# Optimization experiments

Hardware: AMD Instinct MI355X
Metric: run time of the kernel (lower is better)

The kernel has to match this reference:

```python
import jax, jax.numpy as jnp
import numpy as np

B, S, D = 4, 4096, 64

def setup_inputs() -> dict:
    key = jax.random.key(0)
    k1, k2, k3 = jax.random.split(key, 3)
    inputs = jax.random.normal(k1, (B, S, D), dtype=jnp.float32)
    rotation = jax.random.normal(k2, (D, D), dtype=jnp.float32)
    entangle = jax.random.normal(k3, (D, D), dtype=jnp.float32)
    return {"inputs": inputs, "rotation": rotation, "entangle": entangle}

def reference(inputs, rotation, entangle):
    # query/key projections: [B,S,D] @ [D,D] -> [B,S,D]
    query = jnp.einsum('bsd,de->bse', inputs, rotation)
    key = jnp.einsum('bsd,de->bse', inputs, entangle)
    scale = 1.0 / jnp.sqrt(jnp.float32(inputs.shape[-1]))
    # scores: [B,S,S] softmax over last axis
    scores = jax.nn.softmax(jnp.einsum('bqd,bkd->bqk', query, key) * scale, axis=-1)
    # values are the raw inputs (no value projection)
    return jnp.einsum('bqk,bkd->bqd', scores, inputs)
```

## Files before the change

### kernel.cpp

```cpp
#include <hip/hip_runtime.h>
#include <hip/hip_fp16.h>

#define BB 4
#define SS 4096
#define DD 64
#define NSPLIT 4
#define KT_PER (SS / 64 / NSPLIT)

typedef _Float16 half8 __attribute__((ext_vector_type(8)));
typedef _Float16 half4 __attribute__((ext_vector_type(4)));
typedef __fp16 fp16x2 __attribute__((ext_vector_type(2)));
typedef float floatx4 __attribute__((ext_vector_type(4)));

__global__ __launch_bounds__(256) void proj_kernel(
    const float* __restrict__ X, const float* __restrict__ R, const float* __restrict__ E,
    _Float16* __restrict__ Qhi, _Float16* __restrict__ Qlo,
    _Float16* __restrict__ Khi, _Float16* __restrict__ Klo,
    _Float16* __restrict__ Vt)
{
    __shared__ float Rs[64][64];
    __shared__ float Es[64][64];
    __shared__ float Xs[16][68];
    int t = threadIdx.x;
    long rowbase = (long)blockIdx.x * 16;

    for (int j = 0; j < 4; ++j) {
        int idx = j * 256 + t;
        int r = idx >> 4;
        int c = (idx & 15) * 4;
        *(float4*)&Rs[r][c] = ((const float4*)R)[idx];
        *(float4*)&Es[r][c] = ((const float4*)E)[idx];
    }
    *(float4*)&Xs[t >> 4][(t & 15) * 4] = ((const float4*)(X + rowbase * 64))[t];
    __syncthreads();

    int row = t >> 4;
    int c0 = (t & 15) * 4;
    float q[4] = {0.f, 0.f, 0.f, 0.f}, k[4] = {0.f, 0.f, 0.f, 0.f};
#pragma unroll 4
    for (int d = 0; d < 64; ++d) {
        float x = Xs[row][d];
        float4 rv = *(const float4*)&Rs[d][c0];
        float4 ev = *(const float4*)&Es[d][c0];
        q[0] = fmaf(x, rv.x, q[0]); q[1] = fmaf(x, rv.y, q[1]);
        q[2] = fmaf(x, rv.z, q[2]); q[3] = fmaf(x, rv.w, q[3]);
        k[0] = fmaf(x, ev.x, k[0]); k[1] = fmaf(x, ev.y, k[1]);
        k[2] = fmaf(x, ev.z, k[2]); k[3] = fmaf(x, ev.w, k[3]);
    }
    long gq = (rowbase + row) * 64 + c0;
    half4 qh, ql, kh, kl;
    for (int j = 0; j < 4; ++j) {
        _Float16 h = (_Float16)q[j];
        qh[j] = h; ql[j] = (_Float16)(q[j] - (float)h);
        h = (_Float16)k[j];
        kh[j] = h; kl[j] = (_Float16)(k[j] - (float)h);
    }
    *(half4*)(Qhi + gq) = qh; *(half4*)(Qlo + gq) = ql;
    *(half4*)(Khi + gq) = kh; *(half4*)(Klo + gq) = kl;

    int d = t >> 2;
    int si = (t & 3) * 4;
    int b = (int)(rowbase >> 12);
    int sbase = (int)(rowbase & 4095);
    half4 v;
    for (int j = 0; j < 4; ++j) v[j] = (_Float16)Xs[si + j][d];
    *(half4*)(Vt + ((long)(b * 64 + d)) * SS + sbase + si) = v;
}

#define L2E 1.44269504088896340736f
#define PD 72

__global__ __launch_bounds__(256, 4) void attn_partial(
    const _Float16* __restrict__ Qhi, const _Float16* __restrict__ Qlo,
    const _Float16* __restrict__ Khi, const _Float16* __restrict__ Klo,
    const _Float16* __restrict__ Vt,
    float* __restrict__ Op, float* __restrict__ Mp, float* __restrict__ Lp)
{
    __shared__ _Float16 Ksh[64][PD];
    __shared__ _Float16 Ksl[64][PD];
    __shared__ _Float16 Vs[64][PD];
    __shared__ _Float16 Ps[4][16][PD];

    int t = threadIdx.x;
    int wave = t >> 6;
    int lane = t & 63;
    int l15 = lane & 15;
    int quad = lane >> 4;
    int split = blockIdx.y;
    int b = blockIdx.z;
    int q0 = blockIdx.x * 64 + wave * 16;

    long qrow = ((long)b * SS + q0 + l15) * DD;
    half8 qa0h = *(const half8*)(Qhi + qrow + quad * 8);
    half8 qa1h = *(const half8*)(Qhi + qrow + 32 + quad * 8);
    half8 qa0l = *(const half8*)(Qlo + qrow + quad * 8);
    half8 qa1l = *(const half8*)(Qlo + qrow + 32 + quad * 8);

    floatx4 o[4];
    for (int i = 0; i < 4; ++i) o[i] = (floatx4){0.f, 0.f, 0.f, 0.f};
    float m_q = -1e30f;
    float l_q = 0.f;

    const float scale = 0.125f * L2E;

    int rr = t >> 2;
    int cc = (t & 3) * 16;
    long kbase = ((long)b * SS + rr) * DD + cc;
    long vbase = ((long)b * 64 + rr) * SS + cc;

    int kt = split * KT_PER;
    uint4 rh0, rh1, rl0, rl1, rv0, rv1;
    {
        const uint4* khsrc = (const uint4*)(Khi + kbase + (long)kt * 64 * DD);
        rh0 = khsrc[0]; rh1 = khsrc[1];
        const uint4* klsrc = (const uint4*)(Klo + kbase + (long)kt * 64 * DD);
        rl0 = klsrc[0]; rl1 = klsrc[1];
        const uint4* vsrc = (const uint4*)(Vt + vbase + kt * 64);
        rv0 = vsrc[0]; rv1 = vsrc[1];
    }

    for (int i = 0; i < KT_PER; ++i) {
        if (i > 0) __syncthreads();
        {
            uint4* khdst = (uint4*)&Ksh[rr][cc];
            khdst[0] = rh0; khdst[1] = rh1;
            uint4* kldst = (uint4*)&Ksl[rr][cc];
            kldst[0] = rl0; kldst[1] = rl1;
            uint4* vdst = (uint4*)&Vs[rr][cc];
            vdst[0] = rv0; vdst[1] = rv1;
        }
        __syncthreads();

        int ktn = (i + 1 < KT_PER) ? (kt + 1) : kt;
        {
            const uint4* khsrc = (const uint4*)(Khi + kbase + (long)ktn * 64 * DD);
            rh0 = khsrc[0]; rh1 = khsrc[1];
            const uint4* klsrc = (const uint4*)(Klo + kbase + (long)ktn * 64 * DD);
            rl0 = klsrc[0]; rl1 = klsrc[1];
            const uint4* vsrc = (const uint4*)(Vt + vbase + ktn * 64);
            rv0 = vsrc[0]; rv1 = vsrc[1];
        }
        kt = ktn;

        floatx4 s[4];
        for (int ct = 0; ct < 4; ++ct) {
            floatx4 acc = {0.f, 0.f, 0.f, 0.f};
            half8 ka0h = *(const half8*)&Ksh[ct * 16 + l15][quad * 8];
            half8 ka1h = *(const half8*)&Ksh[ct * 16 + l15][32 + quad * 8];
            half8 ka0l = *(const half8*)&Ksl[ct * 16 + l15][quad * 8];
            half8 ka1l = *(const half8*)&Ksl[ct * 16 + l15][32 + quad * 8];
            acc = __builtin_amdgcn_mfma_f32_16x16x32_f16(ka0h, qa0h, acc, 0, 0, 0);
            acc = __builtin_amdgcn_mfma_f32_16x16x32_f16(ka1h, qa1h, acc, 0, 0, 0);
            acc = __builtin_amdgcn_mfma_f32_16x16x32_f16(ka0h, qa0l, acc, 0, 0, 0);
            acc = __builtin_amdgcn_mfma_f32_16x16x32_f16(ka1h, qa1l, acc, 0, 0, 0);
            acc = __builtin_amdgcn_mfma_f32_16x16x32_f16(ka0l, qa0h, acc, 0, 0, 0);
            acc = __builtin_amdgcn_mfma_f32_16x16x32_f16(ka1l, qa1h, acc, 0, 0, 0);
            s[ct] = acc;
        }

        float mt = s[0][0];
        for (int ct = 0; ct < 4; ++ct)
            for (int r = 0; r < 4; ++r)
                mt = fmaxf(mt, s[ct][r]);
        mt = fmaxf(mt, __shfl_xor(mt, 16));
        mt = fmaxf(mt, __shfl_xor(mt, 32));
        mt *= scale;
        float mn = fmaxf(m_q, mt);
        float alpha = exp2f(m_q - mn);
        m_q = mn;

        float rs = 0.f;
        for (int ct = 0; ct < 4; ++ct) {
            float p0 = exp2f(s[ct][0] * scale - mn);
            float p1 = exp2f(s[ct][1] * scale - mn);
            float p2 = exp2f(s[ct][2] * scale - mn);
            float p3 = exp2f(s[ct][3] * scale - mn);
            rs += (p0 + p1) + (p2 + p3);
            union { fp16x2 h2[2]; half4 h4; } u;
            u.h2[0] = __builtin_amdgcn_cvt_pkrtz(p0, p1);
            u.h2[1] = __builtin_amdgcn_cvt_pkrtz(p2, p3);
            *(half4*)&Ps[wave][l15][ct * 16 + quad * 4] = u.h4;
        }
        rs += __shfl_xor(rs, 16);
        rs += __shfl_xor(rs, 32);
        l_q = l_q * alpha + rs;

        for (int r = 0; r < 4; ++r) {
            float a = __shfl(alpha, quad * 4 + r);
            o[0][r] *= a; o[1][r] *= a; o[2][r] *= a; o[3][r] *= a;
        }

        for (int h = 0; h < 2; ++h) {
            half8 pa = *(const half8*)&Ps[wave][l15][h * 32 + quad * 8];
            for (int dt = 0; dt < 4; ++dt) {
                half8 vb = *(const half8*)&Vs[dt * 16 + l15][h * 32 + quad * 8];
                o[dt] = __builtin_amdgcn_mfma_f32_16x16x32_f16(pa, vb, o[dt], 0, 0, 0);
            }
        }
    }

    long pbase = ((long)b * NSPLIT + split) * SS;
    for (int r = 0; r < 4; ++r) {
        int q = q0 + quad * 4 + r;
        long orow = (pbase + q) * DD;
        for (int dt = 0; dt < 4; ++dt)
            Op[orow + dt * 16 + l15] = o[dt][r];
    }
    if (quad == 0) {
        Mp[pbase + q0 + l15] = m_q;
        Lp[pbase + q0 + l15] = l_q;
    }
}

__global__ __launch_bounds__(256) void combine_kernel(
    const float* __restrict__ Op, const float* __restrict__ Mp,
    const float* __restrict__ Lp, float* __restrict__ Out)
{
    int t = threadIdx.x;
    int qi = t >> 4;
    int d4 = (t & 15) * 4;
    long gq = (long)blockIdx.x * 16 + qi;
    int b = (int)(gq >> 12);
    int s = (int)(gq & 4095);

    float m = -1e30f;
    for (int i = 0; i < NSPLIT; ++i)
        m = fmaxf(m, Mp[((long)b * NSPLIT + i) * SS + s]);
    float l = 0.f;
    float4 o = {0.f, 0.f, 0.f, 0.f};
    for (int i = 0; i < NSPLIT; ++i) {
        long pb = ((long)b * NSPLIT + i) * SS + s;
        float a = exp2f(Mp[pb] - m);
        l = fmaf(Lp[pb], a, l);
        float4 oi = *(const float4*)(Op + pb * DD + d4);
        o.x = fmaf(oi.x, a, o.x); o.y = fmaf(oi.y, a, o.y);
        o.z = fmaf(oi.z, a, o.z); o.w = fmaf(oi.w, a, o.w);
    }
    float inv = 1.f / l;
    float4 r = {o.x * inv, o.y * inv, o.z * inv, o.w * inv};
    *(float4*)(Out + gq * DD + d4) = r;
}

extern "C" void kernel_launch(void* const* d_in, const int* in_sizes, int n_in,
                              void* d_out, int out_size, void* d_ws, size_t ws_size,
                              hipStream_t stream) {
    const float* X = (const float*)d_in[0];
    const float* R = (const float*)d_in[1];
    const float* E = (const float*)d_in[2];
    float* Out = (float*)d_out;

    const size_t N = (size_t)BB * SS * DD;
    _Float16* Qhi = (_Float16*)d_ws;
    _Float16* Qlo = Qhi + N;
    _Float16* Khi = Qlo + N;
    _Float16* Klo = Khi + N;
    _Float16* Vt  = Klo + N;
    float* Op = (float*)(Vt + N);
    float* Mp = Op + (size_t)BB * NSPLIT * SS * DD;
    float* Lp = Mp + (size_t)BB * NSPLIT * SS;

    proj_kernel<<<dim3(BB * SS / 16), 256, 0, stream>>>(X, R, E, Qhi, Qlo, Khi, Klo, Vt);
    attn_partial<<<dim3(SS / 64, NSPLIT, BB), 256, 0, stream>>>(Qhi, Qlo, Khi, Klo, Vt, Op, Mp, Lp);
    combine_kernel<<<dim3(BB * SS / 16), 256, 0, stream>>>(Op, Mp, Lp, Out);
}
```

Measured before the change: 120.8 us.

## Rewrite attention kernel with 32x32 MFMA, register-resident K/V and lazy rescale

Replaces the LDS-staged 16x16x32 MFMA attention kernel with one where each wave handles 32 queries using 32x32x16 MFMAs. K and V fragments are loaded straight from global memory into registers and prefetched, so the shared-memory staging and block barriers are gone. P is rearranged between lanes with permlane32_swap instead of a round trip through LDS. The online-softmax rescale is skipped unless the running max grows by more than a threshold, and block indices are remapped so that each XCD works on the same batch and split for better L2 locality. The cost is much higher register pressure and lower occupancy (launch bound 2), plus each wave now fetches K/V from global/L2 redundantly instead of sharing one tile per block.

```diff
diff --git a/kernel.cpp b/kernel.cpp
--- a/kernel.cpp
+++ b/kernel.cpp
@@ -11,6 +11,7 @@
 typedef _Float16 half4 __attribute__((ext_vector_type(4)));
 typedef __fp16 fp16x2 __attribute__((ext_vector_type(2)));
 typedef float floatx4 __attribute__((ext_vector_type(4)));
+typedef float floatx16 __attribute__((ext_vector_type(16)));
 
 __global__ __launch_bounds__(256) void proj_kernel(
     const float* __restrict__ X, const float* __restrict__ R, const float* __restrict__ E,
@@ -68,147 +69,160 @@
 }
 
 #define L2E 1.44269504088896340736f
-#define PD 72
-
-__global__ __launch_bounds__(256, 4) void attn_partial(
+
+__global__ __launch_bounds__(256, 2) void attn_partial(
     const _Float16* __restrict__ Qhi, const _Float16* __restrict__ Qlo,
     const _Float16* __restrict__ Khi, const _Float16* __restrict__ Klo,
     const _Float16* __restrict__ Vt,
     float* __restrict__ Op, float* __restrict__ Mp, float* __restrict__ Lp)
 {
-    __shared__ _Float16 Ksh[64][PD];
-    __shared__ _Float16 Ksl[64][PD];
-    __shared__ _Float16 Vs[64][PD];
-    __shared__ _Float16 Ps[4][16][PD];
-
     int t = threadIdx.x;
     int wave = t >> 6;
     int lane = t & 63;
-    int l15 = lane & 15;
-    int quad = lane >> 4;
-    int split = blockIdx.y;
-    int b = blockIdx.z;
-    int q0 = blockIdx.x * 64 + wave * 16;
-
-    long qrow = ((long)b * SS + q0 + l15) * DD;
-    half8 qa0h = *(const half8*)(Qhi + qrow + quad * 8);
-    half8 qa1h = *(const half8*)(Qhi + qrow + 32 + quad * 8);
-    half8 qa0l = *(const half8*)(Qlo + qrow + quad * 8);
-    half8 qa1l = *(const half8*)(Qlo + qrow + 32 + quad * 8);
-
-    floatx4 o[4];
-    for (int i = 0; i < 4; ++i) o[i] = (floatx4){0.f, 0.f, 0.f, 0.f};
-    float m_q = -1e30f;
-    float l_q = 0.f;
+    int col = lane & 31;
+    int h = lane >> 5;
+
+    int lin = blockIdx.x;
+    int xcd = lin & 7;
+    int idx = lin >> 3;
+    int pair = xcd * 2 + (idx >> 5);
+    int qt = idx & 31;
+    int b = pair >> 2;
+    int split = pair & 3;
+
+    int q0w = qt * 128 + wave * 32;
 
     const float scale = 0.125f * L2E;
 
-    int rr = t >> 2;
-    int cc = (t & 3) * 16;
-    long kbase = ((long)b * SS + rr) * DD + cc;
-    long vbase = ((long)b * 64 + rr) * SS + cc;
-
-    int kt = split * KT_PER;
-    uint4 rh0, rh1, rl0, rl1, rv0, rv1;
-    {
-        const uint4* khsrc = (const uint4*)(Khi + kbase + (long)kt * 64 * DD);
-        rh0 = khsrc[0]; rh1 = khsrc[1];
-        const uint4* klsrc = (const uint4*)(Klo + kbase + (long)kt * 64 * DD);
-        rl0 = klsrc[0]; rl1 = klsrc[1];
-        const uint4* vsrc = (const uint4*)(Vt + vbase + kt * 64);
-        rv0 = vsrc[0]; rv1 = vsrc[1];
-    }
-
-    for (int i = 0; i < KT_PER; ++i) {
-        if (i > 0) __syncthreads();
-        {
-            uint4* khdst = (uint4*)&Ksh[rr][cc];
-            khdst[0] = rh0; khdst[1] = rh1;
-            uint4* kldst = (uint4*)&Ksl[rr][cc];
-            kldst[0] = rl0; kldst[1] = rl1;
-            uint4* vdst = (uint4*)&Vs[rr][cc];
-            vdst[0] = rv0; vdst[1] = rv1;
-        }
-        __syncthreads();
-
-        int ktn = (i + 1 < KT_PER) ? (kt + 1) : kt;
-        {
-            const uint4* khsrc = (const uint4*)(Khi + kbase + (long)ktn * 64 * DD);
-            rh0 = khsrc[0]; rh1 = khsrc[1];
-            const uint4* klsrc = (const uint4*)(Klo + kbase + (long)ktn * 64 * DD);
-            rl0 = klsrc[0]; rl1 = klsrc[1];
-            const uint4* vsrc = (const uint4*)(Vt + vbase + ktn * 64);
-            rv0 = vsrc[0]; rv1 = vsrc[1];
-        }
-        kt = ktn;
-
-        floatx4 s[4];
-        for (int ct = 0; ct < 4; ++ct) {
-            floatx4 acc = {0.f, 0.f, 0.f, 0.f};
-            half8 ka0h = *(const half8*)&Ksh[ct * 16 + l15][quad * 8];
-            half8 ka1h = *(const half8*)&Ksh[ct * 16 + l15][32 + quad * 8];
-            half8 ka0l = *(const half8*)&Ksl[ct * 16 + l15][quad * 8];
-            half8 ka1l = *(const half8*)&Ksl[ct * 16 + l15][32 + quad * 8];
-            acc = __builtin_amdgcn_mfma_f32_16x16x32_f16(ka0h, qa0h, acc, 0, 0, 0);
-            acc = __builtin_amdgcn_mfma_f32_16x16x32_f16(ka1h, qa1h, acc, 0, 0, 0);
-            acc = __builtin_amdgcn_mfma_f32_16x16x32_f16(ka0h, qa0l, acc, 0, 0, 0);
-            acc = __builtin_amdgcn_mfma_f32_16x16x32_f16(ka1h, qa1l, acc, 0, 0, 0);
-            acc = __builtin_amdgcn_mfma_f32_16x16x32_f16(ka0l, qa0h, acc, 0, 0, 0);
-            acc = __builtin_amdgcn_mfma_f32_16x16x32_f16(ka1l, qa1h, acc, 0, 0, 0);
-            s[ct] = acc;
+    long qbase = ((long)b * SS + q0w + col) * DD + h * 8;
+    half8 qh[4], ql[4];
+#pragma unroll
+    for (int dc = 0; dc < 4; ++dc) {
+        qh[dc] = *(const half8*)(Qhi + qbase + dc * 16);
+        ql[dc] = *(const half8*)(Qlo + qbase + dc * 16);
+    }
+
+    int kt0 = split * KT_PER;
+    long koff = ((long)b * SS + (long)kt0 * 64 + col) * DD + h * 8;
+    long voff = ((long)b * 64 + col) * SS + kt0 * 64 + h * 8;
+
+    half8 kh[2][4], kl[2][4], vb[4][2];
+#pragma unroll
+    for (int kb = 0; kb < 2; ++kb)
+#pragma unroll
+        for (int dc = 0; dc < 4; ++dc) {
+            kh[kb][dc] = *(const half8*)(Khi + koff + kb * 32 * DD + dc * 16);
+            kl[kb][dc] = *(const half8*)(Klo + koff + kb * 32 * DD + dc * 16);
+        }
+#pragma unroll
+    for (int kc = 0; kc < 4; ++kc)
+#pragma unroll
+        for (int db = 0; db < 2; ++db)
+            vb[kc][db] = *(const half8*)(Vt + voff + (long)db * 32 * SS + kc * 16);
+
+    floatx16 o0 = {}, o1 = {};
+    float m_q = -1e30f, l_q = 0.f;
+
+#pragma unroll 1
+    for (int it = 0; it < KT_PER; ++it) {
+        floatx16 s[2] = {};
+#pragma unroll
+        for (int dc = 0; dc < 4; ++dc) {
+            s[0] = __builtin_amdgcn_mfma_f32_32x32x16_f16(kh[0][dc], qh[dc], s[0], 0, 0, 0);
+            s[1] = __builtin_amdgcn_mfma_f32_32x32x16_f16(kh[1][dc], qh[dc], s[1], 0, 0, 0);
+            s[0] = __builtin_amdgcn_mfma_f32_32x32x16_f16(kh[0][dc], ql[dc], s[0], 0, 0, 0);
+            s[1] = __builtin_amdgcn_mfma_f32_32x32x16_f16(kh[1][dc], ql[dc], s[1], 0, 0, 0);
+            s[0] = __builtin_amdgcn_mfma_f32_32x32x16_f16(kl[0][dc], qh[dc], s[0], 0, 0, 0);
+            s[1] = __builtin_amdgcn_mfma_f32_32x32x16_f16(kl[1][dc], qh[dc], s[1], 0, 0, 0);
         }
 
         float mt = s[0][0];
-        for (int ct = 0; ct < 4; ++ct)
-            for (int r = 0; r < 4; ++r)
-                mt = fmaxf(mt, s[ct][r]);
-        mt = fmaxf(mt, __shfl_xor(mt, 16));
+#pragma unroll
+        for (int r = 1; r < 16; ++r) mt = fmaxf(mt, s[0][r]);
+#pragma unroll
+        for (int r = 0; r < 16; ++r) mt = fmaxf(mt, s[1][r]);
         mt = fmaxf(mt, __shfl_xor(mt, 32));
         mt *= scale;
-        float mn = fmaxf(m_q, mt);
-        float alpha = exp2f(m_q - mn);
-        m_q = mn;
+
+        if (!__all(mt <= m_q + 8.f)) {
+            float mn = fmaxf(m_q, mt);
+            float alpha = exp2f(m_q - mn);
+            m_q = mn;
+            l_q *= alpha;
+#pragma unroll
+            for (int r = 0; r < 16; ++r) {
+                float a = __shfl(alpha, (r & 3) + 8 * (r >> 2) + 4 * h);
+                o0[r] *= a; o1[r] *= a;
+            }
+        }
 
         float rs = 0.f;
-        for (int ct = 0; ct < 4; ++ct) {
-            float p0 = exp2f(s[ct][0] * scale - mn);
-            float p1 = exp2f(s[ct][1] * scale - mn);
-            float p2 = exp2f(s[ct][2] * scale - mn);
-            float p3 = exp2f(s[ct][3] * scale - mn);
-            rs += (p0 + p1) + (p2 + p3);
-            union { fp16x2 h2[2]; half4 h4; } u;
-            u.h2[0] = __builtin_amdgcn_cvt_pkrtz(p0, p1);
-            u.h2[1] = __builtin_amdgcn_cvt_pkrtz(p2, p3);
-            *(half4*)&Ps[wave][l15][ct * 16 + quad * 4] = u.h4;
-        }
-        rs += __shfl_xor(rs, 16);
+        unsigned int c0[2][4], c1[2][4];
+#pragma unroll
+        for (int kb = 0; kb < 2; ++kb)
+#pragma unroll
+            for (int g = 0; g < 4; ++g) {
+                float p0 = exp2f(s[kb][4 * g + 0] * scale - m_q);
+                float p1 = exp2f(s[kb][4 * g + 1] * scale - m_q);
+                float p2 = exp2f(s[kb][4 * g + 2] * scale - m_q);
+                float p3 = exp2f(s[kb][4 * g + 3] * scale - m_q);
+                rs += (p0 + p1) + (p2 + p3);
+                union { fp16x2 h2; unsigned int u; } u01, u23;
+                u01.h2 = __builtin_amdgcn_cvt_pkrtz(p0, p1);
+                u23.h2 = __builtin_amdgcn_cvt_pkrtz(p2, p3);
+                c0[kb][g] = u01.u;
+                c1[kb][g] = u23.u;
+            }
         rs += __shfl_xor(rs, 32);
-        l_q = l_q * alpha + rs;
-
-        for (int r = 0; r < 4; ++r) {
-            float a = __shfl(alpha, quad * 4 + r);
-            o[0][r] *= a; o[1][r] *= a; o[2][r] *= a; o[3][r] *= a;
-        }
-
-        for (int h = 0; h < 2; ++h) {
-            half8 pa = *(const half8*)&Ps[wave][l15][h * 32 + quad * 8];
-            for (int dt = 0; dt < 4; ++dt) {
-                half8 vb = *(const half8*)&Vs[dt * 16 + l15][h * 32 + quad * 8];
-                o[dt] = __builtin_amdgcn_mfma_f32_16x16x32_f16(pa, vb, o[dt], 0, 0, 0);
+        l_q += rs;
+
+        long kadv = (it + 1 < KT_PER) ? (long)64 * DD : 0;
+        koff += kadv;
+#pragma unroll
+        for (int kb = 0; kb < 2; ++kb)
+#pragma unroll
+            for (int dc = 0; dc < 4; ++dc) {
+                kh[kb][dc] = *(const half8*)(Khi + koff + kb * 32 * DD + dc * 16);
+                kl[kb][dc] = *(const half8*)(Klo + koff + kb * 32 * DD + dc * 16);
             }
-        }
+
+#pragma unroll
+        for (int kc = 0; kc < 4; ++kc) {
+            int kb = kc >> 1;
+            int ge = (kc & 1) * 2;
+            unsigned int a0 = c0[kb][ge], b0 = c0[kb][ge + 1];
+            unsigned int a1 = c1[kb][ge], b1 = c1[kb][ge + 1];
+            auto r0 = __builtin_amdgcn_permlane32_swap(a0, b0, false, false);
+            auto r1 = __builtin_amdgcn_permlane32_swap(a1, b1, false, false);
+            union { unsigned int u[4]; half8 h8; } pa;
+            pa.u[0] = (unsigned int)r0[0];
+            pa.u[1] = (unsigned int)r1[0];
+            pa.u[2] = (unsigned int)r0[1];
+            pa.u[3] = (unsigned int)r1[1];
+            o0 = __builtin_amdgcn_mfma_f32_32x32x16_f16(pa.h8, vb[kc][0], o0, 0, 0, 0);
+            o1 = __builtin_amdgcn_mfma_f32_32x32x16_f16(pa.h8, vb[kc][1], o1, 0, 0, 0);
+        }
+
+        long vadv = (it + 1 < KT_PER) ? 64 : 0;
+        voff += vadv;
+#pragma unroll
+        for (int kc = 0; kc < 4; ++kc)
+#pragma unroll
+            for (int db = 0; db < 2; ++db)
+                vb[kc][db] = *(const half8*)(Vt + voff + (long)db * 32 * SS + kc * 16);
     }
 
     long pbase = ((long)b * NSPLIT + split) * SS;
-    for (int r = 0; r < 4; ++r) {
-        int q = q0 + quad * 4 + r;
-        long orow = (pbase + q) * DD;
-        for (int dt = 0; dt < 4; ++dt)
-            Op[orow + dt * 16 + l15] = o[dt][r];
-    }
-    if (quad == 0) {
-        Mp[pbase + q0 + l15] = m_q;
-        Lp[pbase + q0 + l15] = l_q;
+    long obase = (pbase + q0w) * DD + col;
+#pragma unroll
+    for (int r = 0; r < 16; ++r) {
+        long qrow = (r & 3) + 8 * (r >> 2) + 4 * h;
+        Op[obase + qrow * DD]      = o0[r];
+        Op[obase + qrow * DD + 32] = o1[r];
+    }
+    if (lane < 32) {
+        Mp[pbase + q0w + col] = m_q;
+        Lp[pbase + q0w + col] = l_q;
     }
 }
 
@@ -260,6 +274,6 @@
     float* Lp = Mp + (size_t)BB * NSPLIT * SS;
 
     proj_kernel<<<dim3(BB * SS / 16), 256, 0, stream>>>(X, R, E, Qhi, Qlo, Khi, Klo, Vt);
-    attn_partial<<<dim3(SS / 64, NSPLIT, BB), 256, 0, stream>>>(Qhi, Qlo, Khi, Klo, Vt, Op, Mp, Lp);
+    attn_partial<<<dim3(BB * NSPLIT * (SS / 128)), 256, 0, stream>>>(Qhi, Qlo, Khi, Klo, Vt, Op, Mp, Lp);
     combine_kernel<<<dim3(BB * SS / 16), 256, 0, stream>>>(Op, Mp, Lp, Out);
 }
```

Result: slower. 164.9 us (+36.5%).
